# Kernel tuning notes

Hardware: AMD Instinct MI355X
Metric: run time of the kernel (lower is better)

Reference implementation:

```python
import jax, jax.numpy as jnp
import numpy as np

NUM_RELATION = 7

def setup_inputs() -> dict:
    key = jax.random.key(0)
    ks = jax.random.split(key, 12)
    N, E, D, DO, R, DE = 20000, 640000, 512, 512, NUM_RELATION, 59
    inp = {
        "node_feat": jax.random.normal(ks[0], (N, D), dtype=jnp.float32),
        "edge_weight": jax.random.uniform(ks[1], (E,), dtype=jnp.float32),
        "edge_feat": jax.random.normal(ks[2], (E, DE), dtype=jnp.float32),
        "W_lin": jax.random.normal(ks[3], (DO, R * D), dtype=jnp.float32) * 0.02,
        "b_lin": jax.random.normal(ks[4], (DO,), dtype=jnp.float32) * 0.02,
        "W_self": jax.random.normal(ks[5], (DO, D), dtype=jnp.float32) * 0.02,
        "b_self": jax.random.normal(ks[6], (DO,), dtype=jnp.float32) * 0.02,
        "W_edge": jax.random.normal(ks[7], (DO, DE), dtype=jnp.float32) * 0.02,
        "b_edge": jax.random.normal(ks[8], (DO,), dtype=jnp.float32) * 0.02,
        "node_in": jax.random.randint(ks[9], (E,), 0, N, dtype=jnp.int64) if jax.config.jax_enable_x64 else jax.random.randint(ks[9], (E,), 0, N).astype(jnp.int32),
        "node_out": jax.random.randint(ks[10], (E,), 0, N).astype(jnp.int32),
        "relation": jax.random.randint(ks[11], (E,), 0, R).astype(jnp.int32),
    }
    inp["node_in"] = inp["node_in"].astype(jnp.int32)
    return inp


def reference(node_feat, edge_weight, edge_feat, W_lin, b_lin, W_self, b_self,
              W_edge, b_edge, node_in, node_out, relation):
    N, D = node_feat.shape
    R = NUM_RELATION
    # segment id: node_out * R + relation  (column index in sparse (N, N*R) adjacency)
    seg = node_out * R + relation  # [E]
    # update = adjacency.T @ input  == scatter-add of weighted source features
    msg = node_feat[node_in] * edge_weight[:, None]               # [E, D]
    update = jax.ops.segment_sum(msg, seg, num_segments=N * R)    # [N*R, D]
    # edge_linear path: edge_update scattered with the same segment ids
    edge_msg = (edge_feat @ W_edge.T + b_edge) * edge_weight[:, None]  # [E, D]
    update = update + jax.ops.segment_sum(edge_msg, seg, num_segments=N * R)
    update = update.reshape(N, R * D)                             # [N, R*D]
    # combine: linear(update) + self_loop(input), then relu
    out = update @ W_lin.T + b_lin + node_feat @ W_self.T + b_self
    return jax.nn.relu(out)
```

## Files before the change

### kernel.cpp

```cpp
#include <hip/hip_runtime.h>
#include <stdint.h>

typedef unsigned short u16;
typedef __attribute__((ext_vector_type(8))) __bf16 bf16x8;
typedef __attribute__((ext_vector_type(4))) float f32x4;

#define NREL 7
#define DIM  512
#define DEDGE 59
#define KC   420
#define KCP  448
#define KTOT 4544

__device__ __forceinline__ float bf2f(u16 u) {
  union { unsigned u; float f; } c; c.u = ((unsigned)u) << 16; return c.f;
}
__device__ __forceinline__ u16 f2bf(float f) {
  union { float f; unsigned u; } c; c.f = f;
  unsigned r = ((c.u >> 16) & 1u) + 0x7FFFu;
  return (u16)((c.u + r) >> 16);
}

__device__ __forceinline__ void gload16(const void* g, void* l) {
  __builtin_amdgcn_global_load_lds(
      (__attribute__((address_space(1))) void*)g,
      (__attribute__((address_space(3))) void*)l, 16, 0, 0);
}

__global__ void convA(const float* __restrict__ in, u16* __restrict__ out, int total4) {
  int i = blockIdx.x * 256 + threadIdx.x;
  if (i >= total4) return;
  float4 v = ((const float4*)in)[i];
  ushort4 r;
  r.x = f2bf(v.x); r.y = f2bf(v.y); r.z = f2bf(v.z); r.w = f2bf(v.w);
  ((ushort4*)out)[i] = r;
}

__global__ void buildBW(const float* __restrict__ W_lin, const float* __restrict__ W_self,
                        u16* __restrict__ Bfull, int total4) {
  int gid = blockIdx.x * 256 + threadIdx.x;
  if (gid >= total4) return;
  int idx = gid * 4;
  int o = idx >> 12;
  int k = idx & 4095;
  const float* src = (k < NREL * DIM) ? (W_lin + (size_t)o * (NREL * DIM) + k)
                                      : (W_self + (size_t)o * DIM + (k - NREL * DIM));
  float4 v = *(const float4*)src;
  ushort4 rr;
  rr.x = f2bf(v.x); rr.y = f2bf(v.y); rr.z = f2bf(v.z); rr.w = f2bf(v.w);
  *(ushort4*)(Bfull + (size_t)o * KTOT + k) = rr;
}

__global__ __launch_bounds__(512) void buildCx(const float* __restrict__ W_edge,
                                               const float* __restrict__ b_edge,
                                               const float* __restrict__ W_lin,
                                               u16* __restrict__ Bfull) {
  int c = blockIdx.x;
  int o = threadIdx.x;
  u16* dst = Bfull + (size_t)o * KTOT + NREL * DIM + DIM;
  if (c >= KC) { dst[c] = 0; return; }
  __shared__ float col[DIM];
  int r;
  if (c < NREL * DEDGE) {
    r = c / DEDGE;
    int de = c - r * DEDGE;
    col[o] = W_edge[(size_t)o * DEDGE + de];
  } else {
    r = c - NREL * DEDGE;
    col[o] = b_edge[o];
  }
  __syncthreads();
  const float* wrow = W_lin + (size_t)o * (NREL * DIM) + (size_t)r * DIM;
  float acc = 0.f;
#pragma unroll 8
  for (int d = 0; d < DIM; ++d) acc += col[d] * wrow[d];
  dst[c] = f2bf(acc);
}

__global__ void countK2(const int* __restrict__ node_out, const int* __restrict__ relation,
                        int* __restrict__ counts2, int E) {
  int e = blockIdx.x * 256 + threadIdx.x;
  if (e < E) atomicAdd(&counts2[node_out[e] * 8 + relation[e]], 1);
}

__global__ void scanNode(const int* __restrict__ counts2, int* __restrict__ counts, int N) {
  int n = blockIdx.x * 256 + threadIdx.x;
  if (n >= N) return;
  int s = 0;
#pragma unroll
  for (int r = 0; r < NREL; ++r) s += counts2[n * 8 + r];
  counts[n] = s;
}

__global__ __launch_bounds__(1024) void scanK(const int* __restrict__ counts,
                                              int* __restrict__ offs, int n) {
  __shared__ int lds[1024];
  int tid = threadIdx.x;
  int carry = 0;
  for (int base = 0; base < n; base += 1024) {
    int i = base + tid;
    int v = (i < n) ? counts[i] : 0;
    lds[tid] = v;
    __syncthreads();
    for (int o = 1; o < 1024; o <<= 1) {
      int t = (tid >= o) ? lds[tid - o] : 0;
      __syncthreads();
      lds[tid] += t;
      __syncthreads();
    }
    int excl = lds[tid] - v;
    if (i < n) offs[i] = carry + excl;
    int total = lds[1023];
    carry += total;
    __syncthreads();
  }
  if (tid == 0) offs[n] = carry;
}

__global__ void offs2K(const int* __restrict__ offs, const int* __restrict__ counts2,
                       int* __restrict__ offs2, int* __restrict__ cursor2, int N) {
  int n = blockIdx.x * 256 + threadIdx.x;
  if (n >= N) return;
  int base = offs[n];
#pragma unroll
  for (int r = 0; r < NREL; ++r) {
    offs2[n * 8 + r] = base;
    cursor2[n * 8 + r] = base;
    base += counts2[n * 8 + r];
  }
  offs2[n * 8 + 7] = base;
}

__global__ void fillK2(const int* __restrict__ node_in, const int* __restrict__ node_out,
                       const int* __restrict__ relation, const float* __restrict__ ew,
                       int* __restrict__ cursor2, int* __restrict__ eids,
                       uint2* __restrict__ pairs, int E) {
  int e = blockIdx.x * 256 + threadIdx.x;
  if (e >= E) return;
  int p = atomicAdd(&cursor2[node_out[e] * 8 + relation[e]], 1);
  eids[p] = e;
  pairs[p] = make_uint2((unsigned)node_in[e], __float_as_uint(ew[e]));
}

__global__ __launch_bounds__(64) void gatherG2(const float* __restrict__ ef,
                                               const int* __restrict__ eids,
                                               const uint2* __restrict__ pairs,
                                               const int* __restrict__ offs2,
                                               u16* __restrict__ Mfull) {
  int n = blockIdx.x;
  int lane = threadIdx.x;
  u16* row = Mfull + (size_t)n * KTOT + NREL * DIM + DIM;
  int base = n * 8;
  for (int r = 0; r < NREL; ++r) {
    int p0 = offs2[base + r], p1 = offs2[base + r + 1];
    float acc = 0.f;
    for (int p = p0; p < p1; ++p) {
      int e = __builtin_amdgcn_readfirstlane(eids[p]);
      float w = __uint_as_float(__builtin_amdgcn_readfirstlane(pairs[p].y));
      float v = (lane < DEDGE) ? ef[(size_t)e * DEDGE + lane] : 1.0f;
      acc += w * v;
    }
    if (lane < DEDGE) row[r * DEDGE + lane] = f2bf(acc);
    else if (lane == DEDGE) row[NREL * DEDGE + r] = f2bf(acc);
  }
  if (lane >= 60) {
    for (int c = KC + (lane - 60); c < KCP; c += 4) row[c] = 0;
  }
}

__global__ __launch_bounds__(128) void aggK(const u16* __restrict__ NF,
                                            const uint2* __restrict__ pairs,
                                            const int* __restrict__ offs2,
                                            u16* __restrict__ Mfull) {
  int n = blockIdx.x;
  int o0 = threadIdx.x * 4;
  u16* mrow = Mfull + (size_t)n * KTOT;
  *(ushort4*)(mrow + NREL * DIM + o0) = *(const ushort4*)(NF + (size_t)n * DIM + o0);
  int base = n * 8;
  for (int r = 0; r < NREL; ++r) {
    int p0 = offs2[base + r], p1 = offs2[base + r + 1];
    float a0 = 0.f, a1 = 0.f, a2 = 0.f, a3 = 0.f;
    for (int p = p0; p < p1; ++p) {
      uint2 pr = pairs[p];
      int src = __builtin_amdgcn_readfirstlane((int)pr.x);
      float w = __uint_as_float(__builtin_amdgcn_readfirstlane(pr.y));
      ushort4 hv = *(const ushort4*)(NF + (size_t)src * DIM + o0);
      a0 += w * bf2f(hv.x);
      a1 += w * bf2f(hv.y);
      a2 += w * bf2f(hv.z);
      a3 += w * bf2f(hv.w);
    }
    ushort4 st;
    st.x = f2bf(a0); st.y = f2bf(a1); st.z = f2bf(a2); st.w = f2bf(a3);
    *(ushort4*)(mrow + r * DIM + o0) = st;
  }
}

__global__ __launch_bounds__(256) void gemm_br(const u16* __restrict__ A,
                                               const u16* __restrict__ Bt,
                                               const float* __restrict__ b_lin,
                                               const float* __restrict__ b_self,
                                               float* __restrict__ Cout, int M) {
  __shared__ __align__(16) u16 sA[128 * 32];
  __shared__ __align__(16) u16 sB[128 * 32];
  const int tid = threadIdx.x;
  const int w = tid >> 6, l = tid & 63;
  const int lr = l & 15, kg = l >> 4;
  const int m0 = blockIdx.y * 128, n0 = blockIdx.x * 128;
  const int wr = w >> 1, wc = w & 1;
  f32x4 acc[4][4];
  const f32x4 z4 = {0.f, 0.f, 0.f, 0.f};
#pragma unroll
  for (int i = 0; i < 4; ++i)
#pragma unroll
    for (int j = 0; j < 4; ++j) acc[i][j] = z4;

  const int ktiles = KTOT / 32;
  for (int kt = 0; kt < ktiles; ++kt) {
    const int k0 = kt * 32;
#pragma unroll
    for (int t = 0; t < 2; ++t) {
      int idx = w * 128 + t * 64 + l;
      int row = idx >> 2, kp = idx & 3;
      int gm = m0 + row; gm = gm < M ? gm : M - 1;
      gload16(A + (size_t)gm * KTOT + k0 + kp * 8,
              (char*)sA + (size_t)(w * 128 + t * 64) * 16);
    }
#pragma unroll
    for (int t = 0; t < 2; ++t) {
      int idx = w * 128 + t * 64 + l;
      int row = idx >> 2, kp = idx & 3;
      gload16(Bt + (size_t)(n0 + row) * KTOT + k0 + kp * 8,
              (char*)sB + (size_t)(w * 128 + t * 64) * 16);
    }
    __syncthreads();
    bf16x8 af[4], bfr[4];
#pragma unroll
    for (int i = 0; i < 4; ++i)
      af[i] = *(const bf16x8*)(sA + (size_t)(wr * 64 + i * 16 + lr) * 32 + kg * 8);
#pragma unroll
    for (int j = 0; j < 4; ++j)
      bfr[j] = *(const bf16x8*)(sB + (size_t)(wc * 64 + j * 16 + lr) * 32 + kg * 8);
#pragma unroll
    for (int i = 0; i < 4; ++i)
#pragma unroll
      for (int j = 0; j < 4; ++j)
        acc[i][j] = __builtin_amdgcn_mfma_f32_16x16x32_bf16(af[i], bfr[j], acc[i][j], 0, 0, 0);
    __syncthreads();
  }
#pragma unroll
  for (int i = 0; i < 4; ++i) {
#pragma unroll
    for (int j = 0; j < 4; ++j) {
      int gj = n0 + wc * 64 + j * 16 + lr;
      float bias = b_lin[gj] + b_self[gj];
#pragma unroll
      for (int v = 0; v < 4; ++v) {
        int gm = m0 + wr * 64 + i * 16 + kg * 4 + v;
        if (gm < M)
          ((float*)Cout)[(size_t)gm * DIM + gj] = fmaxf(acc[i][j][v] + bias, 0.f);
      }
    }
  }
}

extern "C" void kernel_launch(void* const* d_in, const int* in_sizes, int n_in,
                              void* d_out, int out_size, void* d_ws, size_t ws_size,
                              hipStream_t stream) {
  const float* node_feat = (const float*)d_in[0];
  const float* edge_weight = (const float*)d_in[1];
  const float* edge_feat = (const float*)d_in[2];
  const float* W_lin = (const float*)d_in[3];
  const float* b_lin = (const float*)d_in[4];
  const float* W_self = (const float*)d_in[5];
  const float* b_self = (const float*)d_in[6];
  const float* W_edge = (const float*)d_in[7];
  const float* b_edge = (const float*)d_in[8];
  const int* node_in = (const int*)d_in[9];
  const int* node_out = (const int*)d_in[10];
  const int* relation = (const int*)d_in[11];
  float* out = (float*)d_out;

  const int N = in_sizes[0] / DIM;
  const int E = in_sizes[1];

  char* ws = (char*)d_ws;
  size_t off = 0;
  auto take = [&](size_t b) {
    char* p = ws + off;
    off += (b + 255) & ~(size_t)255;
    return p;
  };
  u16* NF      = (u16*)take((size_t)N * DIM * 2);
  u16* Bfull   = (u16*)take((size_t)DIM * KTOT * 2);
  u16* Mfull   = (u16*)take((size_t)N * KTOT * 2);
  int* counts2 = (int*)take((size_t)N * 8 * 4);
  int* counts  = (int*)take((size_t)N * 4);
  int* offs    = (int*)take((size_t)(N + 1) * 4);
  int* offs2   = (int*)take((size_t)N * 8 * 4);
  int* cursor2 = (int*)take((size_t)N * 8 * 4);
  int* eids    = (int*)take((size_t)E * 4);
  uint2* pairs = (uint2*)take((size_t)E * 8);
  if (off > ws_size) return;

  hipMemsetAsync(counts2, 0, (size_t)N * 8 * 4, stream);

  {
    int total4 = N * DIM / 4;
    convA<<<(total4 + 255) / 256, 256, 0, stream>>>(node_feat, NF, total4);
  }
  {
    int total4 = DIM * 4096 / 4;
    buildBW<<<(total4 + 255) / 256, 256, 0, stream>>>(W_lin, W_self, Bfull, total4);
  }
  buildCx<<<KCP, 512, 0, stream>>>(W_edge, b_edge, W_lin, Bfull);

  countK2<<<(E + 255) / 256, 256, 0, stream>>>(node_out, relation, counts2, E);
  scanNode<<<(N + 255) / 256, 256, 0, stream>>>(counts2, counts, N);
  scanK<<<1, 1024, 0, stream>>>(counts, offs, N);
  offs2K<<<(N + 255) / 256, 256, 0, stream>>>(offs, counts2, offs2, cursor2, N);
  fillK2<<<(E + 255) / 256, 256, 0, stream>>>(node_in, node_out, relation, edge_weight,
                                              cursor2, eids, pairs, E);

  gatherG2<<<N, 64, 0, stream>>>(edge_feat, eids, pairs, offs2, Mfull);
  aggK<<<N, 128, 0, stream>>>(NF, pairs, offs2, Mfull);

  gemm_br<<<dim3(DIM / 128, (N + 127) / 128), 256, 0, stream>>>(
      Mfull, Bfull, b_lin, b_self, out, N);
}
```

Baseline: 530.6 us.

## Double-buffer GEMM shared tiles and remap blocks into grouped panels

```diff
diff --git a/kernel.cpp b/kernel.cpp
--- a/kernel.cpp
+++ b/kernel.cpp
@@ -201,12 +201,26 @@
                                                const float* __restrict__ b_lin,
                                                const float* __restrict__ b_self,
                                                float* __restrict__ Cout, int M) {
-  __shared__ __align__(16) u16 sA[128 * 32];
-  __shared__ __align__(16) u16 sB[128 * 32];
+  __shared__ __align__(16) u16 sA[2][128 * 32];
+  __shared__ __align__(16) u16 sB[2][128 * 32];
   const int tid = threadIdx.x;
   const int w = tid >> 6, l = tid & 63;
   const int lr = l & 15, kg = l >> 4;
-  const int m0 = blockIdx.y * 128, n0 = blockIdx.x * 128;
+
+  const int id = blockIdx.x;
+  const int npan = gridDim.x >> 2;
+  const int nfull = (npan >> 3) << 3;
+  int p, c;
+  if (id < nfull * 4) {
+    int g = id >> 5, r = id & 31;
+    p = g * 8 + (r & 7);
+    c = r >> 3;
+  } else {
+    int t = id - nfull * 4;
+    p = nfull + (t >> 2);
+    c = t & 3;
+  }
+  const int m0 = p * 128, n0 = c * 128;
   const int wr = w >> 1, wc = w & 1;
   f32x4 acc[4][4];
   const f32x4 z4 = {0.f, 0.f, 0.f, 0.f};
@@ -216,7 +230,8 @@
     for (int j = 0; j < 4; ++j) acc[i][j] = z4;
 
   const int ktiles = KTOT / 32;
-  for (int kt = 0; kt < ktiles; ++kt) {
+
+  auto stage = [&](int kt, int b) {
     const int k0 = kt * 32;
 #pragma unroll
     for (int t = 0; t < 2; ++t) {
@@ -224,23 +239,30 @@
       int row = idx >> 2, kp = idx & 3;
       int gm = m0 + row; gm = gm < M ? gm : M - 1;
       gload16(A + (size_t)gm * KTOT + k0 + kp * 8,
-              (char*)sA + (size_t)(w * 128 + t * 64) * 16);
+              (char*)sA[b] + (size_t)(w * 128 + t * 64) * 16);
     }
 #pragma unroll
     for (int t = 0; t < 2; ++t) {
       int idx = w * 128 + t * 64 + l;
       int row = idx >> 2, kp = idx & 3;
       gload16(Bt + (size_t)(n0 + row) * KTOT + k0 + kp * 8,
-              (char*)sB + (size_t)(w * 128 + t * 64) * 16);
-    }
-    __syncthreads();
+              (char*)sB[b] + (size_t)(w * 128 + t * 64) * 16);
+    }
+  };
+
+  stage(0, 0);
+  __syncthreads();
+
+  for (int kt = 0; kt < ktiles; ++kt) {
+    const int cur = kt & 1;
+    if (kt + 1 < ktiles) stage(kt + 1, cur ^ 1);
     bf16x8 af[4], bfr[4];
 #pragma unroll
     for (int i = 0; i < 4; ++i)
-      af[i] = *(const bf16x8*)(sA + (size_t)(wr * 64 + i * 16 + lr) * 32 + kg * 8);
+      af[i] = *(const bf16x8*)(sA[cur] + (size_t)(wr * 64 + i * 16 + lr) * 32 + kg * 8);
 #pragma unroll
     for (int j = 0; j < 4; ++j)
-      bfr[j] = *(const bf16x8*)(sB + (size_t)(wc * 64 + j * 16 + lr) * 32 + kg * 8);
+      bfr[j] = *(const bf16x8*)(sB[cur] + (size_t)(wc * 64 + j * 16 + lr) * 32 + kg * 8);
 #pragma unroll
     for (int i = 0; i < 4; ++i)
 #pragma unroll
@@ -325,6 +347,8 @@
   gatherG2<<<N, 64, 0, stream>>>(edge_feat, eids, pairs, offs2, Mfull);
   aggK<<<N, 128, 0, stream>>>(NF, pairs, offs2, Mfull);
 
-  gemm_br<<<dim3(DIM / 128, (N + 127) / 128), 256, 0, stream>>>(
-      Mfull, Bfull, b_lin, b_self, out, N);
-}
+  {
+    int npan = (N + 127) / 128;
+    gemm_br<<<npan * 4, 256, 0, stream>>>(Mfull, Bfull, b_lin, b_self, out, N);
+  }
+}
```

After: 527.9 us. No clear change (-0.5%).
